# Kernel optimization log

Hardware: AMD Instinct MI355X
Metric: run time of the kernel (lower is better)

## Reference

```python
import jax, jax.numpy as jnp
import numpy as np
import math


def _conv(x, w, scale, bias, stride=1):
    # Ultralytics-style Conv: Conv2d(bias=False, pad=k//2) + BatchNorm (folded into
    # per-channel scale/bias) + SiLU
    k = w.shape[-1]
    p = k // 2
    y = jax.lax.conv_general_dilated(x, w, (stride, stride), [(p, p), (p, p)],
                                     dimension_numbers=('NCHW', 'OIHW', 'NCHW'))
    y = y * scale[None, :, None, None] + bias[None, :, None, None]
    return y * jax.nn.sigmoid(y)


def setup_inputs() -> dict:
    key = jax.random.key(0)
    ks = jax.random.split(key, 24)
    B, CH1, CH2, H1, W1, HW = 32, 512, 512, 20, 20, 40
    EMB = 256
    s = 0.05
    half = CH1 // 2
    d = {}
    d['x1'] = jax.random.normal(ks[0], (B, CH1, H1, W1), jnp.float32)
    d['x2'] = jax.random.normal(ks[1], (B, CH2, HW, HW), jnp.float32)
    # CrossAttention params
    d['q_w'] = jax.random.normal(ks[2], (EMB, CH1, 3, 3)) * s
    d['q_s'] = 1.0 + jax.random.normal(ks[3], (EMB,)) * s
    d['q_b'] = jax.random.normal(ks[4], (EMB,)) * s
    d['key_w'] = jax.random.normal(ks[5], (EMB, CH2)) * s
    # MGFAB / CSHA params (CA = channel-MLP sigmoid gate, rate=4)
    d['ca_w1'] = jax.random.normal(ks[6], (half // 4, half)) * s
    d['ca_b1'] = jnp.zeros((half // 4,))
    d['ca_w2'] = jax.random.normal(ks[7], (half, half // 4)) * s
    d['ca_b2'] = jnp.zeros((half,))
    d['sa1_w'] = jax.random.normal(ks[8], (half, half, 3, 3)) * s
    d['sa1_s'] = 1.0 + jax.random.normal(ks[9], (half,)) * s
    d['sa1_b'] = jax.random.normal(ks[10], (half,)) * s
    d['sa2_w'] = jax.random.normal(ks[11], (half, half, 3, 3)) * s
    d['sa2_s'] = 1.0 + jax.random.normal(ks[12], (half,)) * s
    d['sa2_b'] = jax.random.normal(ks[13], (half,)) * s
    d['conv2_w'] = jax.random.normal(ks[14], (CH1, 3 * half, 1, 1)) * s
    d['conv2_s'] = 1.0 + jax.random.normal(ks[15], (CH1,)) * s
    d['conv2_b'] = jax.random.normal(ks[16], (CH1,)) * s
    # conv3 branch (single Conv since patch_size[0] < 5)
    d['c3_w'] = jax.random.normal(ks[17], (CH2, CH2, 3, 3)) * s
    d['c3_s'] = 1.0 + jax.random.normal(ks[18], (CH2,)) * s
    d['c3_b'] = jax.random.normal(ks[19], (CH2,)) * s
    return d


def _forward(x1, x2, q_w, q_s, q_b, key_w, ca_w1, ca_b1, ca_w2, ca_b2,
             sa1_w, sa1_s, sa1_b, sa2_w, sa2_s, sa2_b,
             conv2_w, conv2_s, conv2_b, c3_w, c3_s, c3_b):
    NH, PH, PW = 8, 4, 4
    b, c, h, w = x2.shape
    cH = c // NH                       # channels per head
    nph, npw = h // PH, w // PW        # patch grid
    L = nph * npw                      # number of patches == number of q tokens

    # ---- CrossAttention ----
    # value: per-head flattened patches [b*NH, L, cH*PH*PW] (row-major over h,w)
    v = x2.reshape(b * NH, cH, nph, PH, npw, PW).transpose(0, 2, 4, 1, 3, 5)
    v = v.reshape(b * NH, L, cH * PH * PW)
    # key: avg-pool each patch -> linear(c -> emb) -> split heads
    kp = x2.reshape(b, c, nph, PH, npw, PW).mean(axis=(3, 5))  # [b, c, nph, npw]
    k = jnp.einsum('bcl,ec->ble', kp.reshape(b, c, L), key_w)  # [b, L, EMB]
    dh = k.shape[-1] // NH
    k = k.reshape(b, L, NH, dh).transpose(0, 2, 1, 3).reshape(b * NH, L, dh)
    # query: stride-2 conv on x1 -> tokens -> split heads
    q = _conv(x1, q_w, q_s, q_b, stride=2)                     # [b, EMB, nph, npw]
    q = q.reshape(b, -1, L).transpose(0, 2, 1)                 # [b, L, EMB]
    q = q.reshape(b, L, NH, dh).transpose(0, 2, 1, 3).reshape(b * NH, L, dh)
    score = jnp.einsum('nqd,nkd->nqk', q, k) / math.sqrt(dh)
    wts = jax.nn.softmax(score, axis=-1)                       # dropout = identity (eval)
    y = jnp.einsum('nqk,nkv->nqv', wts, v)                     # [b*NH, L, cH*PH*PW]
    # reassemble patches back into [b, c, h, w]
    attn = y.reshape(b, NH, nph, npw, cH, PH, PW).transpose(0, 1, 4, 2, 5, 3, 6)
    attn = attn.reshape(b, c, h, w)

    # ---- conv3 branch with residual ----
    x2_out = _conv(attn, c3_w, c3_s, c3_b) + attn

    x1_up = jnp.repeat(jnp.repeat(x1, 2, axis=2), 2, axis=3)   # [b, ch1, h, w]
    half = x1_up.shape[1] // 2
    a0, a1 = x1_up[:, :half], x1_up[:, half:]
    # CA: channel MLP gate
    xp = a1.transpose(0, 2, 3, 1)                              # [b, h, w, half]
    att = jnp.maximum(xp @ ca_w1.T + ca_b1, 0.0) @ ca_w2.T + ca_b2
    x_ca = a1 * jax.nn.sigmoid(att.transpose(0, 3, 1, 2))
    # SA: two 3x3 Convs + residual
    x_sa = _conv(_conv(x_ca, sa1_w, sa1_s, sa1_b), sa2_w, sa2_s, sa2_b)
    a2 = x_sa + x_ca
    cat = jnp.concatenate([a0, a1, a2], axis=1)                # [b, 3*half, h, w]
    x1_out = _conv(cat, conv2_w, conv2_s, conv2_b)             # [b, ch1, h, w]

    return jnp.concatenate([x1_out, x2_out], axis=1)           # [b, ch1+ch2, h, w]


def reference(x1, x2, q_w, q_s, q_b, key_w, ca_w1, ca_b1, ca_w2, ca_b2,
              sa1_w, sa1_s, sa1_b, sa2_w, sa2_s, sa2_b,
              conv2_w, conv2_s, conv2_b, c3_w, c3_s, c3_b):
    return _forward(x1, x2, q_w, q_s, q_b, key_w, ca_w1, ca_b1, ca_w2, ca_b2,
                    sa1_w, sa1_s, sa1_b, sa2_w, sa2_s, sa2_b,
                    conv2_w, conv2_s, conv2_b, c3_w, c3_s, c3_b)
```

## Files before the change

kernel.cpp:

```cpp
#include <hip/hip_runtime.h>
#include <hip/hip_bf16.h>

using bf16 = __hip_bfloat16;
using bf16x2 = __hip_bfloat162;
typedef __attribute__((ext_vector_type(8))) short short8;
typedef __attribute__((ext_vector_type(4))) float f32x4;

__device__ __forceinline__ float b2f(bf16 v) { return __bfloat162float(v); }
__device__ __forceinline__ bf16 f2b(float v) { return __float2bfloat16(v); }

__device__ __forceinline__ void gload_lds16(const bf16* g, bf16* l)
{
    __builtin_amdgcn_global_load_lds(
        (const __attribute__((address_space(1))) void*)g,
        (__attribute__((address_space(3))) void*)l,
        16, 0, 0);
}

#define PH_BAR() do { __builtin_amdgcn_sched_barrier(0); __builtin_amdgcn_s_barrier(); __builtin_amdgcn_sched_barrier(0); } while (0)
#define WAIT_LGKM0() do { asm volatile("s_waitcnt lgkmcnt(0)" ::: "memory"); __builtin_amdgcn_sched_barrier(0); } while (0)
#define WAIT_VM0() do { asm volatile("s_waitcnt vmcnt(0)" ::: "memory"); __builtin_amdgcn_sched_barrier(0); } while (0)

__global__ __launch_bounds__(256) void nchw_to_nhwc(const float* __restrict__ in,
                                                    bf16* __restrict__ out,
                                                    int C, int H, int W, int pad)
{
    __shared__ bf16 tile[64][68];
    const int S = H * W;
    const int HP = H + 2 * pad, WP = W + 2 * pad;
    const int b = blockIdx.x, s0 = blockIdx.y * 64, c0 = blockIdx.z * 64;
    const int t = threadIdx.x;
    const int a = t & 63, q = t >> 6;
#pragma unroll
    for (int i = 0; i < 16; ++i) {
        int cl = q + i * 4;
        int s = s0 + a;
        tile[cl][a] = (s < S) ? f2b(in[((size_t)b * C + c0 + cl) * S + s]) : f2b(0.f);
    }
    __syncthreads();
#pragma unroll
    for (int i = 0; i < 16; ++i) {
        int sl = q + i * 4;
        int s = s0 + sl;
        if (s < S) {
            int y = s / W, x = s - (s / W) * W;
            out[(((size_t)b * HP + y + pad) * WP + x + pad) * C + c0 + a] = tile[a][sl];
        }
    }
}

__global__ __launch_bounds__(256) void halo_zero(bf16* __restrict__ buf, int W, int C)
{
    const int b = blockIdx.x, y = blockIdx.y;
    const int P = W + 2;
    const bf16 z = f2b(0.f);
    bf16* row = buf + ((size_t)b * P + y) * P * C;
    if (y == 0 || y == P - 1) {
        for (int i = threadIdx.x; i < P * C; i += 256) row[i] = z;
    } else {
        for (int i = threadIdx.x; i < 2 * C; i += 256) {
            const int x = (i < C) ? 0 : P - 1;
            const int c = (i < C) ? i : i - C;
            row[(size_t)x * C + c] = z;
        }
    }
}

__global__ __launch_bounds__(256) void pack_out(const bf16* __restrict__ x1o,
                                                const bf16* __restrict__ x2o,
                                                float* __restrict__ out)
{
    __shared__ bf16 tile[64][68];
    const int b = blockIdx.x, s0 = blockIdx.y * 64, ch0 = blockIdx.z * 64;
    const bf16* src = (ch0 < 512) ? x1o : x2o;
    const int c0 = ch0 & 511;
    const int t = threadIdx.x;
    const int a = t & 63, q = t >> 6;
#pragma unroll
    for (int i = 0; i < 16; ++i) {
        int sl = q + i * 4;
        tile[sl][a] = src[((size_t)b * 1600 + s0 + sl) * 512 + c0 + a];
    }
    __syncthreads();
#pragma unroll
    for (int i = 0; i < 16; ++i) {
        int cl = q + i * 4;
        out[((size_t)b * 1024 + ch0 + cl) * 1600 + s0 + a] = b2f(tile[a][cl]);
    }
}

__global__ __launch_bounds__(256) void reorder_w(const float* __restrict__ w,
                                                 bf16* __restrict__ wr,
                                                 int C, int total)
{
    int i = blockIdx.x * 256 + threadIdx.x;
    if (i >= total) return;
    int nineC = 9 * C;
    int o = i / nineC;
    int r = i - o * nineC;
    int tap = r / C;
    int c = r - tap * C;
    wr[i] = f2b(w[((size_t)o * C + c) * 9 + tap]);
}

__global__ __launch_bounds__(256) void f32_to_bf16(const float* __restrict__ in,
                                                   bf16* __restrict__ out, int n)
{
    int i = blockIdx.x * 256 + threadIdx.x;
    if (i < n) out[i] = f2b(in[i]);
}

__global__ __launch_bounds__(256) void pool_kp(const bf16* __restrict__ x2n,
                                               bf16* __restrict__ kp)
{
    const int p = blockIdx.x;
    const int b = p / 100, l = p - (p / 100) * 100;
    const int ph = l / 10, pw = l - (l / 10) * 10;
    const int t = threadIdx.x;
    const bf16x2* base = (const bf16x2*)(x2n + (((size_t)(b * 40 + ph * 4) * 40) + pw * 4) * 512) + t;
    float sx = 0.f, sy = 0.f;
#pragma unroll
    for (int py = 0; py < 4; ++py)
#pragma unroll
        for (int px = 0; px < 4; ++px) {
            float2 v = __bfloat1622float2(base[(py * 40 + px) * 256]);
            sx += v.x; sy += v.y;
        }
    ((bf16x2*)(kp + (size_t)p * 512))[t] = __float22bfloat162_rn(make_float2(sx * 0.0625f, sy * 0.0625f));
}

__global__ __launch_bounds__(256) void ca_mlp(const bf16* __restrict__ x1n,
                                              const float* __restrict__ w1, const float* __restrict__ b1,
                                              const float* __restrict__ w2, const float* __restrict__ b2,
                                              bf16* __restrict__ xca)
{
    __shared__ float a1v[256];
    __shared__ float part[4][64];
    __shared__ float hid[64];
    const int blk = blockIdx.x;
    const int b = blk / 400;
    const int rem = blk - b * 400;
    const int y = rem / 20, x = rem - (rem / 20) * 20;
    const int t = threadIdx.x;
    const bf16* src = x1n + ((size_t)(b * 22 + y + 1) * 22 + x + 1) * 512 + 256;
    a1v[t] = b2f(src[t]);
    __syncthreads();
    {
        const int h = t & 63, seg = t >> 6;
        float acc = 0.f;
        const float* wp = w1 + (size_t)h * 256 + seg * 64;
        const float* ap = a1v + seg * 64;
#pragma unroll 8
        for (int c = 0; c < 64; ++c) acc += wp[c] * ap[c];
        part[seg][h] = acc;
    }
    __syncthreads();
    if (t < 64)
        hid[t] = fmaxf(part[0][t] + part[1][t] + part[2][t] + part[3][t] + b1[t], 0.f);
    __syncthreads();
    float acc2 = b2[t];
    const float* w2p = w2 + (size_t)t * 64;
#pragma unroll 8
    for (int h = 0; h < 64; ++h) acc2 += w2p[h] * hid[h];
    const float g = 1.f / (1.f + __expf(-acc2));
    const bf16 o = f2b(a1v[t] * g);
    const size_t obase = ((size_t)(b * 42 + 2 * y + 1) * 42 + 2 * x + 1) * 256 + t;
    xca[obase] = o;
    xca[obase + 256] = o;
    xca[obase + 42 * 256] = o;
    xca[obase + 42 * 256 + 256] = o;
}

__global__ __launch_bounds__(256, 1)
void attn_kernel(const float* __restrict__ q, const float* __restrict__ k,
                 const bf16* __restrict__ x2n, bf16* __restrict__ attn)
{
    __shared__ float sc[100][100];
    __shared__ bf16 wT[100][104];
    const int t = threadIdx.x;
    const int n = blockIdx.x;
    const int b = n >> 3, hd = n & 7;
    const float* qn = q + (size_t)n * 3200;
    const float* kn = k + (size_t)n * 3200;
    for (int e = t; e < 10000; e += 256) {
        const int i = e / 100;
        const int j = e - i * 100;
        const float4* qa = (const float4*)(qn + i * 32);
        const float4* ka = (const float4*)(kn + j * 32);
        float d = 0.f;
#pragma unroll
        for (int u = 0; u < 8; ++u) {
            float4 xv = qa[u], yv = ka[u];
            d += xv.x * yv.x + xv.y * yv.y + xv.z * yv.z + xv.w * yv.w;
        }
        sc[i][j] = d * 0.17677669529663687f;
    }
    __syncthreads();
    if (t < 100) {
        float mx = -1e30f;
        for (int j = 0; j < 100; ++j) mx = fmaxf(mx, sc[t][j]);
        float s = 0.f;
        for (int j = 0; j < 100; ++j) s += __expf(sc[t][j] - mx);
        const float inv = 1.f / s;
        for (int j = 0; j < 100; ++j) wT[j][t] = f2b(__expf(sc[t][j] - mx) * inv);
    }
    __syncthreads();
    const int ch0 = (t & 15) * 4;
    const int pix = t >> 4;
    const int py = pix >> 2, px = pix & 3;
    const bf16* vbase = x2n + (((size_t)(b * 40 + py) * 40) + px) * 512 + hd * 64 + ch0;
    for (int ql0 = 0; ql0 < 100; ql0 += 20) {
        float2 a0[20], a1[20];
#pragma unroll
        for (int i = 0; i < 20; ++i) { a0[i] = make_float2(0.f, 0.f); a1[i] = make_float2(0.f, 0.f); }
        for (int l = 0; l < 100; ++l) {
            const int ph = l / 10, pw = l - (l / 10) * 10;
            const bf16* vp = vbase + ((size_t)(ph * 160 + pw * 4)) * 512;
            const float2 v01 = __bfloat1622float2(*(const bf16x2*)vp);
            const float2 v23 = __bfloat1622float2(*(const bf16x2*)(vp + 2));
            const bf16x2* wp = (const bf16x2*)&wT[l][ql0];
#pragma unroll
            for (int ii = 0; ii < 10; ++ii) {
                const float2 w2 = __bfloat1622float2(wp[ii]);
                a0[ii * 2 + 0].x += w2.x * v01.x; a0[ii * 2 + 0].y += w2.x * v01.y;
                a1[ii * 2 + 0].x += w2.x * v23.x; a1[ii * 2 + 0].y += w2.x * v23.y;
                a0[ii * 2 + 1].x += w2.y * v01.x; a0[ii * 2 + 1].y += w2.y * v01.y;
                a1[ii * 2 + 1].x += w2.y * v23.x; a1[ii * 2 + 1].y += w2.y * v23.y;
            }
        }
#pragma unroll
        for (int i = 0; i < 20; ++i) {
            const int ql = ql0 + i;
            const int ph = ql / 10, pw = ql - (ql / 10) * 10;
            bf16* op = attn + (((size_t)(b * 42 + ph * 4 + py + 1) * 42) + pw * 4 + px + 1) * 512 + hd * 64 + ch0;
            *(bf16x2*)op = __float22bfloat162_rn(a0[i]);
            *(bf16x2*)(op + 2) = __float22bfloat162_rn(a1[i]);
        }
    }
}

enum ConvMode { M_QCONV = 0, M_SA1 = 1, M_SA2 = 2, M_C3 = 3, M_CONV2 = 4, M_KPROJ = 5 };

template <int MODE>
__global__ __launch_bounds__(256, 2)
void conv_mfma(const bf16* __restrict__ in, const bf16* __restrict__ wr,
               const float* __restrict__ scale, const float* __restrict__ bias,
               float* __restrict__ outf)
{
    constexpr int CIN  = 512;
    constexpr int TAPS = (MODE == M_KPROJ) ? 1 : 9;
    constexpr int STR  = 2;
    constexpr int HP   = 22;
    constexpr int WOUT = 10;
    constexpr int K    = TAPS * CIN;
    constexpr int KD   = (TAPS == 9) ? 3 : 1;

    __shared__ bf16 Al[128][64];
    __shared__ bf16 Bl[128][64];

    const int t = threadIdx.x;
    const int p0 = blockIdx.x * 128;
    const int n0 = blockIdx.y * 128;

    int s_row[4], s_dst8[4], s_src8[4], s_b[4], s_oy[4], s_ox[4];
    const bf16* bB[4];
#pragma unroll
    for (int i = 0; i < 4; ++i) {
        const int task = t + i * 256;
        const int row = task >> 3, chk = task & 7;
        s_row[i] = row;
        s_dst8[i] = chk * 8;
        s_src8[i] = (chk ^ (row & 7)) * 8;
        const int p = p0 + row;
        const int bb = p / 100;
        const int s = p - bb * 100;
        s_b[i] = bb;
        s_oy[i] = s / WOUT;
        s_ox[i] = s - s_oy[i] * WOUT;
        bB[i] = wr + (size_t)(n0 + row) * K + s_src8[i];
    }

    const bf16* aP1[4];
    if (MODE == M_KPROJ) {
#pragma unroll
        for (int i = 0; i < 4; ++i)
            aP1[i] = in + (size_t)(p0 + s_row[i]) * 512 + s_src8[i];
    }

    const int lane = t & 63;
    const int wv = t >> 6;
    const int m_off = (wv >> 1) * 64;
    const int n_off = (wv & 1) * 64;
    const int fr = lane & 15;
    const int qd = lane >> 4;
    const int xa = (fr & 7) << 4;

    f32x4 acc[4][4];
#pragma unroll
    for (int mi = 0; mi < 4; ++mi)
#pragma unroll
        for (int ni = 0; ni < 4; ++ni)
            acc[mi][ni] = (f32x4){0.f, 0.f, 0.f, 0.f};

    for (int ky = 0; ky < KD; ++ky)
    for (int kx = 0; kx < KD; ++kx) {
        const bf16* aT[4];
        if (TAPS == 9) {
#pragma unroll
            for (int i = 0; i < 4; ++i)
                aT[i] = in + ((size_t)((s_b[i] * HP + s_oy[i] * STR + ky) * HP) + s_ox[i] * STR + kx) * CIN + s_src8[i];
        }
        const int kk0 = (ky * KD + kx) * CIN;
        for (int c0 = 0; c0 < CIN; c0 += 64) {
#pragma unroll
            for (int i = 0; i < 4; ++i) {
                const bf16* sa = (MODE == M_KPROJ) ? (aP1[i] + c0) : (aT[i] + c0);
                gload_lds16(sa, &Al[s_row[i]][s_dst8[i]]);
            }
#pragma unroll
            for (int i = 0; i < 4; ++i)
                gload_lds16(bB[i] + (kk0 + c0), &Bl[s_row[i]][s_dst8[i]]);
            __syncthreads();
#pragma unroll
            for (int ks = 0; ks < 2; ++ks) {
                short8 af[4], bfr[4];
                const int coff = (ks * 64 + qd * 16) ^ xa;
#pragma unroll
                for (int mi = 0; mi < 4; ++mi)
                    af[mi] = *(const short8*)((const char*)&Al[m_off + mi * 16 + fr][0] + coff);
#pragma unroll
                for (int ni = 0; ni < 4; ++ni)
                    bfr[ni] = *(const short8*)((const char*)&Bl[n_off + ni * 16 + fr][0] + coff);
#pragma unroll
                for (int mi = 0; mi < 4; ++mi)
#pragma unroll
                    for (int ni = 0; ni < 4; ++ni)
                        acc[mi][ni] = __builtin_amdgcn_mfma_f32_16x16x32_bf16(af[mi], bfr[ni], acc[mi][ni], 0, 0, 0);
            }
            __syncthreads();
        }
    }

#pragma unroll
    for (int ni = 0; ni < 4; ++ni) {
        const int nn = n0 + n_off + ni * 16 + fr;
        float scv = 1.f, bsv = 0.f;
        if (MODE != M_KPROJ) { scv = scale[nn]; bsv = bias[nn]; }
#pragma unroll
        for (int mi = 0; mi < 4; ++mi) {
            const int mb = p0 + m_off + mi * 16 + qd * 4;
#pragma unroll
            for (int r = 0; r < 4; ++r) {
                const int p = mb + r;
                const float v = acc[mi][ni][r];
                const int bb = p / 100, l = p - (p / 100) * 100;
                if (MODE == M_KPROJ) {
                    outf[(((size_t)(bb * 8 + (nn >> 5))) * 100 + l) * 32 + (nn & 31)] = v;
                } else {
                    const float y = v * scv + bsv;
                    const float a = y / (1.f + __expf(-y));
                    outf[(((size_t)(bb * 8 + (nn >> 5))) * 100 + l) * 32 + (nn & 31)] = a;
                }
            }
        }
    }
}

template <int MODE>
__global__ __launch_bounds__(512, 2)
void conv_mfma256(const bf16* __restrict__ in, const bf16* __restrict__ in2,
                  const bf16* __restrict__ wr,
                  const float* __restrict__ scale, const float* __restrict__ bias,
                  const bf16* __restrict__ resid,
                  bf16* __restrict__ outb)
{
    constexpr int CIN  = (MODE == M_C3) ? 512 : (MODE == M_CONV2 ? 768 : 256);
    constexpr int TAPS = (MODE == M_CONV2) ? 1 : 9;
    constexpr int K    = TAPS * CIN;
    constexpr int NT   = K / 64;
    constexpr int CPT  = CIN / 64;
    constexpr int L2C  = (CPT == 8) ? 3 : 2;
    constexpr int HP   = 42;

    __shared__ bf16 Al[2][256][64];
    __shared__ bf16 Bl[2][256][64];

    const int t = threadIdx.x;
    const int p0 = blockIdx.x * 256;
    const int n0 = blockIdx.y * 256;

    const int row64 = t >> 3;
    const int chk = t & 7;
    const int src8 = (chk ^ (row64 & 7)) * 8;
    const int dst8 = chk * 8;

    const bf16* aBase[4];
    const bf16* aBase2[4];
#pragma unroll
    for (int si = 0; si < 4; ++si) {
        const int p = p0 + si * 64 + row64;
        const int b = p / 1600;
        const int s = p - b * 1600;
        const int oy = s / 40, ox = s - (s / 40) * 40;
        if (MODE == M_CONV2) {
            aBase[si]  = in  + ((size_t)(b * 22 + (oy >> 1) + 1) * 22 + (ox >> 1) + 1) * 512 + src8;
            aBase2[si] = in2 + ((size_t)(b * 1600 + oy * 40 + ox)) * 256 + src8;
        } else {
            aBase[si]  = in  + ((size_t)(b * HP + oy) * HP + ox) * CIN + src8;
            aBase2[si] = nullptr;
        }
    }
    const bf16* bBase[4];
#pragma unroll
    for (int si = 0; si < 4; ++si)
        bBase[si] = wr + (size_t)(n0 + si * 64 + row64) * K + src8;

    const int lane = t & 63;
    const int wv = t >> 6;
    const int m_off = (wv >> 2) * 128;
    const int n_off = (wv & 3) * 64;
    const int fr = lane & 15;
    const int qd = lane >> 4;
    const int xa = (fr & 7) << 4;

    f32x4 acc[8][4];
#pragma unroll
    for (int mi = 0; mi < 8; ++mi)
#pragma unroll
        for (int ni = 0; ni < 4; ++ni)
            acc[mi][ni] = (f32x4){0.f, 0.f, 0.f, 0.f};

#define LDA8(buf, rrow, kkk) \
    (*(const short8*)((const char*)&Al[buf][rrow][0] + ((((kkk) * 64) + qd * 16) ^ xa)))
#define LDB8(buf, rrow, kkk) \
    (*(const short8*)((const char*)&Bl[buf][rrow][0] + ((((kkk) * 64) + qd * 16) ^ xa)))

#pragma unroll
    for (int si = 0; si < 4; ++si)
        gload_lds16(aBase[si], &Al[0][si * 64 + row64][dst8]);
#pragma unroll
    for (int si = 0; si < 4; ++si)
        gload_lds16(bBase[si], &Bl[0][si * 64 + row64][dst8]);
    asm volatile("s_waitcnt vmcnt(0)" ::: "memory");
    __syncthreads();

#pragma clang loop unroll(disable)
    for (int kt = 0; kt < NT; ++kt) {
        const int cur = kt & 1;
        const int nxt = cur ^ 1;
        const int ktn = kt + 1;
        const bool pf = (ktn < NT);
        int offAn = 0, c0n = 0;
        if (pf) {
            if (MODE == M_CONV2) {
                c0n = ktn * 64;
            } else {
                const int tap = ktn >> L2C;
                const int ci = ktn & (CPT - 1);
                const int ky = tap / 3, kx = tap - ky * 3;
                offAn = (ky * HP + kx) * CIN + ci * 64;
            }
        }
        const int offBn = ktn * 64;

        auto stage = [&](int si) {
            if (si < 4) {
                const bf16* sa;
                if (MODE == M_CONV2) sa = (c0n < 512) ? (aBase[si] + c0n) : (aBase2[si] + (c0n - 512));
                else sa = aBase[si] + offAn;
                gload_lds16(sa, &Al[nxt][si * 64 + row64][dst8]);
            } else {
                gload_lds16(bBase[si - 4] + offBn, &Bl[nxt][(si - 4) * 64 + row64][dst8]);
            }
        };

        short8 af[4][2], bf0[2][2], bf1[2][2];

#pragma unroll
        for (int m4 = 0; m4 < 4; ++m4) {
            af[m4][0] = LDA8(cur, m_off + m4 * 16 + fr, 0);
            af[m4][1] = LDA8(cur, m_off + m4 * 16 + fr, 1);
        }
#pragma unroll
        for (int n2 = 0; n2 < 2; ++n2) {
            bf0[n2][0] = LDB8(cur, n_off + n2 * 16 + fr, 0);
            bf0[n2][1] = LDB8(cur, n_off + n2 * 16 + fr, 1);
        }
        if (pf) { stage(0); stage(1); stage(2); }
        PH_BAR();
        WAIT_LGKM0();
        __builtin_amdgcn_s_setprio(1);
#pragma unroll
        for (int m4 = 0; m4 < 4; ++m4)
#pragma unroll
            for (int n2 = 0; n2 < 2; ++n2) {
                acc[m4][n2] = __builtin_amdgcn_mfma_f32_16x16x32_bf16(af[m4][0], bf0[n2][0], acc[m4][n2], 0, 0, 0);
                acc[m4][n2] = __builtin_amdgcn_mfma_f32_16x16x32_bf16(af[m4][1], bf0[n2][1], acc[m4][n2], 0, 0, 0);
            }
        __builtin_amdgcn_s_setprio(0);
        PH_BAR();

#pragma unroll
        for (int n2 = 0; n2 < 2; ++n2) {
            bf1[n2][0] = LDB8(cur, n_off + (2 + n2) * 16 + fr, 0);
            bf1[n2][1] = LDB8(cur, n_off + (2 + n2) * 16 + fr, 1);
        }
        if (pf) { stage(3); stage(4); stage(5); }
        PH_BAR();
        WAIT_LGKM0();
        __builtin_amdgcn_s_setprio(1);
#pragma unroll
        for (int m4 = 0; m4 < 4; ++m4)
#pragma unroll
            for (int n2 = 0; n2 < 2; ++n2) {
                acc[m4][2 + n2] = __builtin_amdgcn_mfma_f32_16x16x32_bf16(af[m4][0], bf1[n2][0], acc[m4][2 + n2], 0, 0, 0);
                acc[m4][2 + n2] = __builtin_amdgcn_mfma_f32_16x16x32_bf16(af[m4][1], bf1[n2][1], acc[m4][2 + n2], 0, 0, 0);
            }
        __builtin_amdgcn_s_setprio(0);
        PH_BAR();

#pragma unroll
        for (int m4 = 0; m4 < 4; ++m4) {
            af[m4][0] = LDA8(cur, m_off + (4 + m4) * 16 + fr, 0);
            af[m4][1] = LDA8(cur, m_off + (4 + m4) * 16 + fr, 1);
        }
        if (pf) { stage(6); stage(7); }
        PH_BAR();
        WAIT_LGKM0();
        __builtin_amdgcn_s_setprio(1);
#pragma unroll
        for (int m4 = 0; m4 < 4; ++m4)
#pragma unroll
            for (int n2 = 0; n2 < 2; ++n2) {
                acc[4 + m4][n2] = __builtin_amdgcn_mfma_f32_16x16x32_bf16(af[m4][0], bf0[n2][0], acc[4 + m4][n2], 0, 0, 0);
                acc[4 + m4][n2] = __builtin_amdgcn_mfma_f32_16x16x32_bf16(af[m4][1], bf0[n2][1], acc[4 + m4][n2], 0, 0, 0);
            }
        __builtin_amdgcn_s_setprio(0);
        PH_BAR();

        __builtin_amdgcn_s_setprio(1);
#pragma unroll
        for (int m4 = 0; m4 < 4; ++m4)
#pragma unroll
            for (int n2 = 0; n2 < 2; ++n2) {
                acc[4 + m4][2 + n2] = __builtin_amdgcn_mfma_f32_16x16x32_bf16(af[m4][0], bf1[n2][0], acc[4 + m4][2 + n2], 0, 0, 0);
                acc[4 + m4][2 + n2] = __builtin_amdgcn_mfma_f32_16x16x32_bf16(af[m4][1], bf1[n2][1], acc[4 + m4][2 + n2], 0, 0, 0);
            }
        __builtin_amdgcn_s_setprio(0);
        WAIT_VM0();
        PH_BAR();
    }
#undef LDA8
#undef LDB8

#pragma unroll
    for (int ni = 0; ni < 4; ++ni) {
        const int nn = n0 + n_off + ni * 16 + fr;
        const float scv = scale[nn];
        const float bsv = bias[nn];
#pragma unroll
        for (int mi = 0; mi < 8; ++mi) {
            const int mb = p0 + m_off + mi * 16 + qd * 4;
#pragma unroll
            for (int r = 0; r < 4; ++r) {
                const int p = mb + r;
                const float y = acc[mi][ni][r] * scv + bsv;
                const float a = y / (1.f + __expf(-y));
                if (MODE == M_SA1) {
                    const int bb = p / 1600; const int s = p - bb * 1600;
                    const int oy = s / 40, ox = s - (s / 40) * 40;
                    outb[(((size_t)(bb * 42 + oy + 1)) * 42 + ox + 1) * 256 + nn] = f2b(a);
                } else if (MODE == M_SA2) {
                    const int bb = p / 1600; const int s = p - bb * 1600;
                    const int oy = s / 40, ox = s - (s / 40) * 40;
                    const size_t roff = (((size_t)(bb * 42 + oy + 1)) * 42 + ox + 1) * 256 + nn;
                    outb[(size_t)p * 256 + nn] = f2b(a + b2f(resid[roff]));
                } else if (MODE == M_C3) {
                    const int bb = p / 1600; const int s = p - bb * 1600;
                    const int oy = s / 40, ox = s - (s / 40) * 40;
                    const size_t roff = (((size_t)(bb * 42 + oy + 1)) * 42 + ox + 1) * 512 + nn;
                    outb[(size_t)p * 512 + nn] = f2b(a + b2f(resid[roff]));
                } else {
                    outb[(size_t)p * 512 + nn] = f2b(a);
                }
            }
        }
    }
}

extern "C" void kernel_launch(void* const* d_in, const int* in_sizes, int n_in,
                              void* d_out, int out_size, void* d_ws, size_t ws_size,
                              hipStream_t stream)
{
    const float* x1      = (const float*)d_in[0];
    const float* x2      = (const float*)d_in[1];
    const float* q_w     = (const float*)d_in[2];
    const float* q_s     = (const float*)d_in[3];
    const float* q_b     = (const float*)d_in[4];
    const float* key_w   = (const float*)d_in[5];
    const float* ca_w1   = (const float*)d_in[6];
    const float* ca_b1   = (const float*)d_in[7];
    const float* ca_w2   = (const float*)d_in[8];
    const float* ca_b2   = (const float*)d_in[9];
    const float* sa1_w   = (const float*)d_in[10];
    const float* sa1_s   = (const float*)d_in[11];
    const float* sa1_b   = (const float*)d_in[12];
    const float* sa2_w   = (const float*)d_in[13];
    const float* sa2_s   = (const float*)d_in[14];
    const float* sa2_b   = (const float*)d_in[15];
    const float* conv2_w = (const float*)d_in[16];
    const float* conv2_s = (const float*)d_in[17];
    const float* conv2_b = (const float*)d_in[18];
    const float* c3_w    = (const float*)d_in[19];
    const float* c3_s    = (const float*)d_in[20];
    const float* c3_b    = (const float*)d_in[21];

    char* ws = (char*)d_ws;
    const size_t o_x1n  = 0;
    const size_t o_x2n  = 15859712;
    const size_t o_attn = 68288512;
    const size_t o_xca  = 126091264;
    const size_t o_tbuf = 154992640;
    const size_t o_a2   = 183894016;
    const size_t o_ws1  = 210108416;
    const size_t o_ws2  = 211288064;
    const size_t o_wc2  = 212467712;
    const size_t o_k    = o_tbuf;
    const size_t o_q    = o_tbuf + 3276800;
    const size_t o_wkey = o_tbuf + 6553600;
    const size_t o_kp   = o_a2;
    const size_t o_wq   = o_a2 + 3276800;
    const size_t o_wc3  = o_xca;

    bf16*  x1n    = (bf16*)(ws + o_x1n);
    bf16*  x2n    = (bf16*)(ws + o_x2n);
    float* k_attn = (float*)(ws + o_k);
    float* q_attn = (float*)(ws + o_q);
    bf16*  attn   = (bf16*)(ws + o_attn);
    bf16*  xca    = (bf16*)(ws + o_xca);
    bf16*  tbuf   = (bf16*)(ws + o_tbuf);
    bf16*  a2     = (bf16*)(ws + o_a2);
    bf16*  wq     = (bf16*)(ws + o_wq);
    bf16*  wc3    = (bf16*)(ws + o_wc3);
    bf16*  wsa1   = (bf16*)(ws + o_ws1);
    bf16*  wsa2   = (bf16*)(ws + o_ws2);
    bf16*  kp     = (bf16*)(ws + o_kp);
    bf16*  wkey   = (bf16*)(ws + o_wkey);
    bf16*  wc2    = (bf16*)(ws + o_wc2);
    bf16*  x2o    = (bf16*)(ws + o_x2n);
    bf16*  x1o    = (bf16*)(ws + o_attn);

    const dim3 blk(256);
    const dim3 blk512(512);

    halo_zero<<<dim3(32, 22), blk, 0, stream>>>(x1n, 20, 512);
    halo_zero<<<dim3(32, 42), blk, 0, stream>>>(xca, 40, 256);
    halo_zero<<<dim3(32, 42), blk, 0, stream>>>(attn, 40, 512);

    nchw_to_nhwc<<<dim3(32, 7, 8), blk, 0, stream>>>(x1, x1n, 512, 20, 20, 1);
    nchw_to_nhwc<<<dim3(32, 25, 8), blk, 0, stream>>>(x2, x2n, 512, 40, 40, 0);
    reorder_w<<<4608, blk, 0, stream>>>(q_w,  wq,   512, 256 * 512 * 9);
    reorder_w<<<2304, blk, 0, stream>>>(sa1_w, wsa1, 256, 256 * 256 * 9);
    reorder_w<<<2304, blk, 0, stream>>>(sa2_w, wsa2, 256, 256 * 256 * 9);
    f32_to_bf16<<<512, blk, 0, stream>>>(key_w, wkey, 256 * 512);
    f32_to_bf16<<<1536, blk, 0, stream>>>(conv2_w, wc2, 512 * 768);
    pool_kp<<<3200, blk, 0, stream>>>(x2n, kp);

    conv_mfma<M_KPROJ><<<dim3(25, 2), blk, 0, stream>>>(kp, wkey, nullptr, nullptr, k_attn);
    conv_mfma<M_QCONV><<<dim3(25, 2), blk, 0, stream>>>(x1n, wq, q_s, q_b, q_attn);

    attn_kernel<<<256, blk, 0, stream>>>(q_attn, k_attn, x2n, attn);

    halo_zero<<<dim3(32, 42), blk, 0, stream>>>(tbuf, 40, 256);

    ca_mlp<<<12800, blk, 0, stream>>>(x1n, ca_w1, ca_b1, ca_w2, ca_b2, xca);

    conv_mfma256<M_SA1><<<dim3(200, 1), blk512, 0, stream>>>(xca, nullptr, wsa1,
        sa1_s, sa1_b, nullptr, tbuf);
    conv_mfma256<M_SA2><<<dim3(200, 1), blk512, 0, stream>>>(tbuf, nullptr, wsa2,
        sa2_s, sa2_b, xca, a2);

    reorder_w<<<9216, blk, 0, stream>>>(c3_w, wc3, 512, 512 * 512 * 9);
    conv_mfma256<M_C3><<<dim3(200, 2), blk512, 0, stream>>>(attn, nullptr, wc3,
        c3_s, c3_b, attn, x2o);
    conv_mfma256<M_CONV2><<<dim3(200, 2), blk512, 0, stream>>>(x1n, a2, wc2,
        conv2_s, conv2_b, nullptr, x1o);

    pack_out<<<dim3(32, 25, 16), blk, 0, stream>>>(x1o, x2o, (float*)d_out);

    (void)in_sizes; (void)n_in; (void)out_size; (void)ws_size;
}
```

Before: 1.473 ms.

## Merge C3 and SA1 convs into one launch and restructure MFMA pipeline

Pulls the 256x256 conv main loop out into a device function and adds a combined kernel that runs the independent C3 conv (400 tiles) and SA1 conv (200 tiles) in a single 600-block grid. The aim is to fill the GPU better and drop one launch and tail. The C3 weight buffer moves to its own workspace region and is reordered early so it no longer aliases xca. The inner loop goes from four MFMA phases to two, holding all four B fragments in registers, and uses partial vmcnt waits (4 and 2) in place of a full drain each iteration. The extra fragments raise register pressure, and the partial waits depend on the exact order in which the loads are issued.

```diff
diff --git a/kernel.cpp b/kernel.cpp
--- a/kernel.cpp
+++ b/kernel.cpp
@@ -20,6 +20,8 @@
 #define PH_BAR() do { __builtin_amdgcn_sched_barrier(0); __builtin_amdgcn_s_barrier(); __builtin_amdgcn_sched_barrier(0); } while (0)
 #define WAIT_LGKM0() do { asm volatile("s_waitcnt lgkmcnt(0)" ::: "memory"); __builtin_amdgcn_sched_barrier(0); } while (0)
 #define WAIT_VM0() do { asm volatile("s_waitcnt vmcnt(0)" ::: "memory"); __builtin_amdgcn_sched_barrier(0); } while (0)
+#define WAIT_VM2() do { asm volatile("s_waitcnt vmcnt(2)" ::: "memory"); __builtin_amdgcn_sched_barrier(0); } while (0)
+#define WAIT_VM4() do { asm volatile("s_waitcnt vmcnt(4)" ::: "memory"); __builtin_amdgcn_sched_barrier(0); } while (0)
 
 __global__ __launch_bounds__(256) void nchw_to_nhwc(const float* __restrict__ in,
                                                     bf16* __restrict__ out,
@@ -367,12 +369,12 @@
 }
 
 template <int MODE>
-__global__ __launch_bounds__(512, 2)
-void conv_mfma256(const bf16* __restrict__ in, const bf16* __restrict__ in2,
-                  const bf16* __restrict__ wr,
-                  const float* __restrict__ scale, const float* __restrict__ bias,
-                  const bf16* __restrict__ resid,
-                  bf16* __restrict__ outb)
+__device__ __forceinline__ void conv_body256(
+    const bf16* __restrict__ in, const bf16* __restrict__ in2,
+    const bf16* __restrict__ wr, const float* __restrict__ scale,
+    const float* __restrict__ bias, const bf16* __restrict__ resid,
+    bf16* __restrict__ outb, bf16* lA, bf16* lB,
+    int mtile, int ntile)
 {
     constexpr int CIN  = (MODE == M_C3) ? 512 : (MODE == M_CONV2 ? 768 : 256);
     constexpr int TAPS = (MODE == M_CONV2) ? 1 : 9;
@@ -382,12 +384,9 @@
     constexpr int L2C  = (CPT == 8) ? 3 : 2;
     constexpr int HP   = 42;
 
-    __shared__ bf16 Al[2][256][64];
-    __shared__ bf16 Bl[2][256][64];
-
     const int t = threadIdx.x;
-    const int p0 = blockIdx.x * 256;
-    const int n0 = blockIdx.y * 256;
+    const int p0 = mtile * 256;
+    const int n0 = ntile * 256;
 
     const int row64 = t >> 3;
     const int chk = t & 7;
@@ -431,16 +430,16 @@
             acc[mi][ni] = (f32x4){0.f, 0.f, 0.f, 0.f};
 
 #define LDA8(buf, rrow, kkk) \
-    (*(const short8*)((const char*)&Al[buf][rrow][0] + ((((kkk) * 64) + qd * 16) ^ xa)))
+    (*(const short8*)((const char*)lA + (buf) * 32768 + (rrow) * 128 + ((((kkk) * 64) + qd * 16) ^ xa)))
 #define LDB8(buf, rrow, kkk) \
-    (*(const short8*)((const char*)&Bl[buf][rrow][0] + ((((kkk) * 64) + qd * 16) ^ xa)))
+    (*(const short8*)((const char*)lB + (buf) * 32768 + (rrow) * 128 + ((((kkk) * 64) + qd * 16) ^ xa)))
 
 #pragma unroll
     for (int si = 0; si < 4; ++si)
-        gload_lds16(aBase[si], &Al[0][si * 64 + row64][dst8]);
+        gload_lds16(aBase[si], lA + (si * 64 + row64) * 64 + dst8);
 #pragma unroll
     for (int si = 0; si < 4; ++si)
-        gload_lds16(bBase[si], &Bl[0][si * 64 + row64][dst8]);
+        gload_lds16(bBase[si], lB + (si * 64 + row64) * 64 + dst8);
     asm volatile("s_waitcnt vmcnt(0)" ::: "memory");
     __syncthreads();
 
@@ -463,18 +462,17 @@
         }
         const int offBn = ktn * 64;
 
-        auto stage = [&](int si) {
-            if (si < 4) {
-                const bf16* sa;
-                if (MODE == M_CONV2) sa = (c0n < 512) ? (aBase[si] + c0n) : (aBase2[si] + (c0n - 512));
-                else sa = aBase[si] + offAn;
-                gload_lds16(sa, &Al[nxt][si * 64 + row64][dst8]);
-            } else {
-                gload_lds16(bBase[si - 4] + offBn, &Bl[nxt][(si - 4) * 64 + row64][dst8]);
-            }
+        auto stA = [&](int si) {
+            const bf16* sa;
+            if (MODE == M_CONV2) sa = (c0n < 512) ? (aBase[si] + c0n) : (aBase2[si] + (c0n - 512));
+            else sa = aBase[si] + offAn;
+            gload_lds16(sa, lA + nxt * 16384 + (si * 64 + row64) * 64 + dst8);
         };
-
-        short8 af[4][2], bf0[2][2], bf1[2][2];
+        auto stB = [&](int si) {
+            gload_lds16(bBase[si] + offBn, lB + nxt * 16384 + (si * 64 + row64) * 64 + dst8);
+        };
+
+        short8 af[4][2], bfr[4][2];
 
 #pragma unroll
         for (int m4 = 0; m4 < 4; ++m4) {
@@ -482,72 +480,43 @@
             af[m4][1] = LDA8(cur, m_off + m4 * 16 + fr, 1);
         }
 #pragma unroll
-        for (int n2 = 0; n2 < 2; ++n2) {
-            bf0[n2][0] = LDB8(cur, n_off + n2 * 16 + fr, 0);
-            bf0[n2][1] = LDB8(cur, n_off + n2 * 16 + fr, 1);
-        }
-        if (pf) { stage(0); stage(1); stage(2); }
+        for (int n4 = 0; n4 < 4; ++n4) {
+            bfr[n4][0] = LDB8(cur, n_off + n4 * 16 + fr, 0);
+            bfr[n4][1] = LDB8(cur, n_off + n4 * 16 + fr, 1);
+        }
+        if (pf) { stA(0); stA(2); stB(0); stB(1); }
         PH_BAR();
         WAIT_LGKM0();
         __builtin_amdgcn_s_setprio(1);
 #pragma unroll
         for (int m4 = 0; m4 < 4; ++m4)
 #pragma unroll
-            for (int n2 = 0; n2 < 2; ++n2) {
-                acc[m4][n2] = __builtin_amdgcn_mfma_f32_16x16x32_bf16(af[m4][0], bf0[n2][0], acc[m4][n2], 0, 0, 0);
-                acc[m4][n2] = __builtin_amdgcn_mfma_f32_16x16x32_bf16(af[m4][1], bf0[n2][1], acc[m4][n2], 0, 0, 0);
+            for (int n4 = 0; n4 < 4; ++n4) {
+                acc[m4][n4] = __builtin_amdgcn_mfma_f32_16x16x32_bf16(af[m4][0], bfr[n4][0], acc[m4][n4], 0, 0, 0);
+                acc[m4][n4] = __builtin_amdgcn_mfma_f32_16x16x32_bf16(af[m4][1], bfr[n4][1], acc[m4][n4], 0, 0, 0);
             }
         __builtin_amdgcn_s_setprio(0);
+        if (pf) { WAIT_VM4(); } else { WAIT_VM0(); }
         PH_BAR();
 
 #pragma unroll
-        for (int n2 = 0; n2 < 2; ++n2) {
-            bf1[n2][0] = LDB8(cur, n_off + (2 + n2) * 16 + fr, 0);
-            bf1[n2][1] = LDB8(cur, n_off + (2 + n2) * 16 + fr, 1);
-        }
-        if (pf) { stage(3); stage(4); stage(5); }
+        for (int m4 = 0; m4 < 4; ++m4) {
+            af[m4][0] = LDA8(cur, m_off + (4 + m4) * 16 + fr, 0);
+            af[m4][1] = LDA8(cur, m_off + (4 + m4) * 16 + fr, 1);
+        }
+        if (pf) { stB(2); stB(3); stA(1); stA(3); }
         PH_BAR();
         WAIT_LGKM0();
         __builtin_amdgcn_s_setprio(1);
 #pragma unroll
         for (int m4 = 0; m4 < 4; ++m4)
 #pragma unroll
-            for (int n2 = 0; n2 < 2; ++n2) {
-                acc[m4][2 + n2] = __builtin_amdgcn_mfma_f32_16x16x32_bf16(af[m4][0], bf1[n2][0], acc[m4][2 + n2], 0, 0, 0);
-                acc[m4][2 + n2] = __builtin_amdgcn_mfma_f32_16x16x32_bf16(af[m4][1], bf1[n2][1], acc[m4][2 + n2], 0, 0, 0);
+            for (int n4 = 0; n4 < 4; ++n4) {
+                acc[4 + m4][n4] = __builtin_amdgcn_mfma_f32_16x16x32_bf16(af[m4][0], bfr[n4][0], acc[4 + m4][n4], 0, 0, 0);
+                acc[4 + m4][n4] = __builtin_amdgcn_mfma_f32_16x16x32_bf16(af[m4][1], bfr[n4][1], acc[4 + m4][n4], 0, 0, 0);
             }
         __builtin_amdgcn_s_setprio(0);
-        PH_BAR();
-
-#pragma unroll
-        for (int m4 = 0; m4 < 4; ++m4) {
-            af[m4][0] = LDA8(cur, m_off + (4 + m4) * 16 + fr, 0);
-            af[m4][1] = LDA8(cur, m_off + (4 + m4) * 16 + fr, 1);
-        }
-        if (pf) { stage(6); stage(7); }
-        PH_BAR();
-        WAIT_LGKM0();
-        __builtin_amdgcn_s_setprio(1);
-#pragma unroll
-        for (int m4 = 0; m4 < 4; ++m4)
-#pragma unroll
-            for (int n2 = 0; n2 < 2; ++n2) {
-                acc[4 + m4][n2] = __builtin_amdgcn_mfma_f32_16x16x32_bf16(af[m4][0], bf0[n2][0], acc[4 + m4][n2], 0, 0, 0);
-                acc[4 + m4][n2] = __builtin_amdgcn_mfma_f32_16x16x32_bf16(af[m4][1], bf0[n2][1], acc[4 + m4][n2], 0, 0, 0);
-            }
-        __builtin_amdgcn_s_setprio(0);
-        PH_BAR();
-
-        __builtin_amdgcn_s_setprio(1);
-#pragma unroll
-        for (int m4 = 0; m4 < 4; ++m4)
-#pragma unroll
-            for (int n2 = 0; n2 < 2; ++n2) {
-                acc[4 + m4][2 + n2] = __builtin_amdgcn_mfma_f32_16x16x32_bf16(af[m4][0], bf1[n2][0], acc[4 + m4][2 + n2], 0, 0, 0);
-                acc[4 + m4][2 + n2] = __builtin_amdgcn_mfma_f32_16x16x32_bf16(af[m4][1], bf1[n2][1], acc[4 + m4][2 + n2], 0, 0, 0);
-            }
-        __builtin_amdgcn_s_setprio(0);
-        WAIT_VM0();
+        if (pf) { WAIT_VM2(); }
         PH_BAR();
     }
 #undef LDA8
@@ -585,6 +554,43 @@
                 }
             }
         }
+    }
+}
+
+template <int MODE>
+__global__ __launch_bounds__(512, 2)
+void conv_mfma256(const bf16* __restrict__ in, const bf16* __restrict__ in2,
+                  const bf16* __restrict__ wr,
+                  const float* __restrict__ scale, const float* __restrict__ bias,
+                  const bf16* __restrict__ resid,
+                  bf16* __restrict__ outb)
+{
+    __shared__ bf16 Al[2][256][64];
+    __shared__ bf16 Bl[2][256][64];
+    int mtile, ntile;
+    if (MODE == M_CONV2 || MODE == M_C3) { mtile = blockIdx.x >> 1; ntile = blockIdx.x & 1; }
+    else { mtile = blockIdx.x; ntile = 0; }
+    conv_body256<MODE>(in, in2, wr, scale, bias, resid, outb,
+                       &Al[0][0][0], &Bl[0][0][0], mtile, ntile);
+}
+
+__global__ __launch_bounds__(512, 2)
+void conv_c3_sa1(const bf16* __restrict__ attn, const bf16* __restrict__ wc3,
+                 const float* __restrict__ c3_s, const float* __restrict__ c3_b,
+                 bf16* __restrict__ x2o,
+                 const bf16* __restrict__ xca, const bf16* __restrict__ wsa1,
+                 const float* __restrict__ sa1_s, const float* __restrict__ sa1_b,
+                 bf16* __restrict__ tbuf)
+{
+    __shared__ bf16 Al[2][256][64];
+    __shared__ bf16 Bl[2][256][64];
+    const int bx = blockIdx.x;
+    if (bx < 400) {
+        conv_body256<M_C3>(attn, nullptr, wc3, c3_s, c3_b, attn, x2o,
+                           &Al[0][0][0], &Bl[0][0][0], bx >> 1, bx & 1);
+    } else {
+        conv_body256<M_SA1>(xca, nullptr, wsa1, sa1_s, sa1_b, nullptr, tbuf,
+                            &Al[0][0][0], &Bl[0][0][0], bx - 400, 0);
     }
 }
 
@@ -630,7 +636,7 @@
     const size_t o_wkey = o_tbuf + 6553600;
     const size_t o_kp   = o_a2;
     const size_t o_wq   = o_a2 + 3276800;
-    const size_t o_wc3  = o_xca;
+    const size_t o_wc3  = o_a2 + 5636096;
 
     bf16*  x1n    = (bf16*)(ws + o_x1n);
     bf16*  x2n    = (bf16*)(ws + o_x2n);
@@ -660,6 +666,7 @@
     nchw_to_nhwc<<<dim3(32, 7, 8), blk, 0, stream>>>(x1, x1n, 512, 20, 20, 1);
     nchw_to_nhwc<<<dim3(32, 25, 8), blk, 0, stream>>>(x2, x2n, 512, 40, 40, 0);
     reorder_w<<<4608, blk, 0, stream>>>(q_w,  wq,   512, 256 * 512 * 9);
+    reorder_w<<<9216, blk, 0, stream>>>(c3_w, wc3,  512, 512 * 512 * 9);
     reorder_w<<<2304, blk, 0, stream>>>(sa1_w, wsa1, 256, 256 * 256 * 9);
     reorder_w<<<2304, blk, 0, stream>>>(sa2_w, wsa2, 256, 256 * 256 * 9);
     f32_to_bf16<<<512, blk, 0, stream>>>(key_w, wkey, 256 * 512);
@@ -675,15 +682,12 @@
 
     ca_mlp<<<12800, blk, 0, stream>>>(x1n, ca_w1, ca_b1, ca_w2, ca_b2, xca);
 
-    conv_mfma256<M_SA1><<<dim3(200, 1), blk512, 0, stream>>>(xca, nullptr, wsa1,
-        sa1_s, sa1_b, nullptr, tbuf);
-    conv_mfma256<M_SA2><<<dim3(200, 1), blk512, 0, stream>>>(tbuf, nullptr, wsa2,
+    conv_c3_sa1<<<600, blk512, 0, stream>>>(attn, wc3, c3_s, c3_b, x2o,
+                                            xca, wsa1, sa1_s, sa1_b, tbuf);
+
+    conv_mfma256<M_SA2><<<200, blk512, 0, stream>>>(tbuf, nullptr, wsa2,
         sa2_s, sa2_b, xca, a2);
-
-    reorder_w<<<9216, blk, 0, stream>>>(c3_w, wc3, 512, 512 * 512 * 9);
-    conv_mfma256<M_C3><<<dim3(200, 2), blk512, 0, stream>>>(attn, nullptr, wc3,
-        c3_s, c3_b, attn, x2o);
-    conv_mfma256<M_CONV2><<<dim3(200, 2), blk512, 0, stream>>>(x1n, a2, wc2,
+    conv_mfma256<M_CONV2><<<400, blk512, 0, stream>>>(x1n, a2, wc2,
         conv2_s, conv2_b, nullptr, x1o);
 
     pack_out<<<dim3(32, 25, 16), blk, 0, stream>>>(x1o, x2o, (float*)d_out);
```

Result: faster. 1.427 ms (-3.1%).
